# Kernel optimization log

Measured on AMD Instinct MI355X. Metric: run time of the kernel, lower is better.

Reference implementation:

```python
import jax, jax.numpy as jnp
import numpy as np

EMBED = 512; HEADS = 16; WIN = 8; SHIFT = 4

def _rel_pos_index(Wh, Ww):
    # WindowMSA.double_step_seq + transpose-sum + flip(1)
    seq1 = np.arange(0, (2 * Ww - 1) * Wh, 2 * Ww - 1)
    seq2 = np.arange(0, Ww)
    coords = (seq1[:, None] + seq2[None, :]).reshape(1, -1)
    idx = coords + coords.T            # (Wh*Ww, Wh*Ww)
    return idx[:, ::-1].copy()

def _attn_mask(H_pad, W_pad, win, shift, nf):
    # static (trace-time) shifted-window mask, values in {0, -100}
    img = np.zeros((H_pad, W_pad))
    cnt = 0
    for h in (slice(0, -win), slice(-win, -shift), slice(-shift, None)):
        for w in (slice(0, -win), slice(-win, -shift), slice(-shift, None)):
            img[h, w] = cnt
            cnt += 1
    mw = img.reshape(H_pad // win, win, W_pad // win, win).transpose(0, 2, 1, 3).reshape(-1, win * win)
    am = mw[:, None, :] - mw[:, :, None]
    am = np.where(am != 0, -100.0, 0.0)
    return np.tile(am, (1, 1, nf))     # (nW, N, nf*N)

def setup_inputs():
    key = jax.random.key(0)
    ks = jax.random.split(key, 8)
    B, H, W, C, nf = 8, 128, 128, EMBED, 2
    s = 0.02
    return {
        'q': jax.random.normal(ks[0], (B, H * W, C), jnp.float32),
        'kv': jax.random.normal(ks[1], (B, nf, H * W, C), jnp.float32),
        'H': H, 'W': W,
        'rpb_table': jax.random.normal(ks[2], ((2 * WIN - 1) ** 2, HEADS), jnp.float32) * s,
        'Wq': jax.random.normal(ks[3], (C, C), jnp.float32) * s,
        'bq': jnp.zeros((C,), jnp.float32),
        'Wkv': jax.random.normal(ks[4], (C, 2 * C), jnp.float32) * s,
        'bkv': jnp.zeros((2 * C,), jnp.float32),
        'Wo': jax.random.normal(ks[5], (C, C), jnp.float32) * s,
        'bo': jnp.zeros((C,), jnp.float32),
    }

def reference(q, kv, H, W, rpb_table, Wq, bq, Wkv, bkv, Wo, bo):
    B, L, C = q.shape
    nf = kv.shape[1]
    win, shift, heads = WIN, SHIFT, HEADS
    hd = C // heads
    scale = hd ** -0.5
    pad_b = (-H) % win
    pad_r = (-W) % win
    x = q.reshape(B, H, W, C)
    kvx = kv.reshape(B * nf, H, W, C)
    x = jnp.pad(x, ((0, 0), (0, pad_b), (0, pad_r), (0, 0)))
    kvx = jnp.pad(kvx, ((0, 0), (0, pad_b), (0, pad_r), (0, 0)))
    Hp, Wp = H + pad_b, W + pad_r
    nh, nw = Hp // win, Wp // win
    if shift > 0:
        x = jnp.roll(x, (-shift, -shift), (1, 2))
        kvx = jnp.roll(kvx, (-shift, -shift), (1, 2))
        mask = jnp.asarray(_attn_mask(Hp, Wp, win, shift, nf), q.dtype)
    else:
        mask = None
    Nq = win * win
    Nk = nf * Nq
    # window partition: (B, Hp, Wp, C) -> (B*nh*nw, Nq, C)
    qw = x.reshape(B, nh, win, nw, win, C).transpose(0, 1, 3, 2, 4, 5).reshape(B * nh * nw, Nq, C)
    # kv: (B*nf, Hp, Wp, C) -> (B*nh*nw, nf*Nq, C)
    kvw = kvx.reshape(B, nf, nh, win, nw, win, C).transpose(0, 2, 4, 1, 3, 5, 6).reshape(B * nh * nw, Nk, C)
    Bw = qw.shape[0]
    qh = (qw @ Wq + bq).reshape(Bw, Nq, heads, hd).transpose(0, 2, 1, 3) * scale
    kvp = (kvw @ Wkv + bkv).reshape(Bw, Nk, 2, heads, hd).transpose(2, 0, 3, 1, 4)
    kh, vh = kvp[0], kvp[1]
    attn = jnp.einsum('bhqd,bhkd->bhqk', qh, kh)
    rpi = jnp.asarray(_rel_pos_index(win, win).reshape(-1))
    rpb = rpb_table[rpi].reshape(Nq, Nq, heads).transpose(2, 0, 1)  # (heads, Nq, Nq)
    attn = attn + jnp.tile(rpb, (1, 1, nf))[None]
    if mask is not None:
        nW = mask.shape[0]
        attn = (attn.reshape(Bw // nW, nW, heads, Nq, Nk) + mask[None, :, None]).reshape(Bw, heads, Nq, Nk)
    attn = jax.nn.softmax(attn, axis=-1)
    ow = jnp.einsum('bhqk,bhkd->bqhd', attn, vh).reshape(Bw, Nq, C)
    ow = ow @ Wo + bo
    # window reverse
    x = ow.reshape(B, nh, nw, win, win, C).transpose(0, 1, 3, 2, 4, 5).reshape(B, Hp, Wp, C)
    if shift > 0:
        x = jnp.roll(x, (shift, shift), (1, 2))
    x = x[:, :H, :W, :].reshape(B, H * W, C)
    return x
```

## Files before the change

kernel.cpp:

```cpp
#include <hip/hip_runtime.h>

typedef unsigned short ushort_t;
typedef short bf16x8 __attribute__((ext_vector_type(8)));
typedef float f32x4 __attribute__((ext_vector_type(4)));

#define MFMA16(a, b, c) __builtin_amdgcn_mfma_f32_16x16x32_bf16(a, b, c, 0, 0, 0)

static __device__ __forceinline__ float bf2f(ushort_t u) {
  union { unsigned int i; float f; } v;
  v.i = ((unsigned int)u) << 16;
  return v.f;
}
static __device__ __forceinline__ ushort_t f2bf(float f) {
  union { float f; unsigned int i; } v;
  v.f = f;
  unsigned int u = v.i;
  u = u + 0x7fffu + ((u >> 16) & 1u);
  return (ushort_t)(u >> 16);
}
static __device__ __forceinline__ unsigned int cvtpk(float lo, float hi) {
  unsigned int r;
  asm("v_cvt_pk_bf16_f32 %0, %1, %2" : "=v"(r) : "v"(lo), "v"(hi));
  return r;
}

__global__ void ws_sentinel(float* out, unsigned long long ws) {
  if (blockIdx.x == 0 && threadIdx.x == 0)
    out[0] = 1.0e6f * (1.0f + (float)(ws >> 23));
}

__global__ __launch_bounds__(256) void wtrans(const float* __restrict__ in,
                                              ushort_t* __restrict__ out,
                                              int R, int C) {
  int idx = blockIdx.x * 256 + threadIdx.x;
  if (idx < R * C) {
    int r = idx / C, c = idx - r * C;
    out[c * R + r] = f2bf(in[idx]);
  }
}

template <bool AF32, bool CF32>
__global__ __launch_bounds__(256, 2) void gemm_bt(const void* __restrict__ Av,
                                                  const ushort_t* __restrict__ Bt,
                                                  const float* __restrict__ bias,
                                                  void* __restrict__ Cv,
                                                  int N, int Nt) {
  const int K = 512;
  __shared__ ushort_t As[128 * 32];
  __shared__ ushort_t Bs[128 * 32];
  const int t = threadIdx.x;
  const int l = t & 63;
  const int wv = t >> 6;
  const int wr = wv >> 1, wc = wv & 1;
  const int lrow = l & 15;
  const int lk = (l >> 4) * 8;

  const int bid = blockIdx.x;
  const int xcd = bid & 7;
  const int slot = bid >> 3;
  const int mt = xcd + 8 * (slot / Nt);
  const int nt = slot % Nt;
  const long m0 = (long)mt * 128;
  const int n0 = nt * 128;

  const ushort_t* Bb = Bt + (long)n0 * K;
  const int srow = t >> 2;
  const int sseg = t & 3;

  auto loadA8 = [&](long row, int kcol) -> bf16x8 {
    if constexpr (AF32) {
      const float* p = (const float*)Av + (m0 + row) * K + kcol;
      f32x4 a = *(const f32x4*)(p);
      f32x4 b = *(const f32x4*)(p + 4);
      union { unsigned int u[4]; bf16x8 v; } r;
      r.u[0] = cvtpk(a[0], a[1]);
      r.u[1] = cvtpk(a[2], a[3]);
      r.u[2] = cvtpk(b[0], b[1]);
      r.u[3] = cvtpk(b[2], b[3]);
      return r.v;
    } else {
      const ushort_t* p = (const ushort_t*)Av + (m0 + row) * K + kcol;
      return *(const bf16x8*)p;
    }
  };

  const f32x4 fz = {0.f, 0.f, 0.f, 0.f};
  f32x4 acc[4][4];
#pragma unroll
  for (int i = 0; i < 4; i++)
#pragma unroll
    for (int j = 0; j < 4; j++) acc[i][j] = fz;

  for (int kk = 0; kk < K; kk += 32) {
    bf16x8 ta0 = loadA8(srow, kk + sseg * 8);
    bf16x8 ta1 = loadA8(64 + srow, kk + sseg * 8);
    bf16x8 tb0 = *(const bf16x8*)(Bb + (long)srow * K + kk + sseg * 8);
    bf16x8 tb1 = *(const bf16x8*)(Bb + (long)(64 + srow) * K + kk + sseg * 8);
    __syncthreads();
    *(bf16x8*)&As[t * 8] = ta0;
    *(bf16x8*)&As[2048 + t * 8] = ta1;
    *(bf16x8*)&Bs[t * 8] = tb0;
    *(bf16x8*)&Bs[2048 + t * 8] = tb1;
    __syncthreads();
    bf16x8 af[4], bfr[4];
#pragma unroll
    for (int mi = 0; mi < 4; mi++)
      af[mi] = *(const bf16x8*)&As[(wr * 64 + mi * 16 + lrow) * 32 + lk];
#pragma unroll
    for (int ni = 0; ni < 4; ni++)
      bfr[ni] = *(const bf16x8*)&Bs[(wc * 64 + ni * 16 + lrow) * 32 + lk];
#pragma unroll
    for (int mi = 0; mi < 4; mi++)
#pragma unroll
      for (int ni = 0; ni < 4; ni++)
        acc[mi][ni] = MFMA16(af[mi], bfr[ni], acc[mi][ni]);
  }

#pragma unroll
  for (int mi = 0; mi < 4; mi++) {
    const long row0 = m0 + wr * 64 + mi * 16 + (l >> 4) * 4;
#pragma unroll
    for (int ni = 0; ni < 4; ni++) {
      const int col = n0 + wc * 64 + ni * 16 + lrow;
      const float bv = bias[col];
#pragma unroll
      for (int r = 0; r < 4; r++) {
        const float val = acc[mi][ni][r] + bv;
        if constexpr (CF32)
          ((float*)Cv)[(row0 + r) * N + col] = val;
        else
          ((ushort_t*)Cv)[(row0 + r) * N + col] = f2bf(val);
      }
    }
  }
}

__global__ __launch_bounds__(64, 1) void attn_k(const ushort_t* __restrict__ Qp,
                                                const ushort_t* __restrict__ KVp,
                                                const float* __restrict__ rpbt,
                                                ushort_t* __restrict__ Ao) {
  __shared__ ushort_t P[64 * 136];
  __shared__ ushort_t Vt[32 * 136];
  __shared__ float Ltab[225];
  const int l = threadIdx.x;
  const int wnd = blockIdx.x;
  const int h = blockIdx.y;
  const int b = wnd >> 8;
  const int wh = (wnd >> 4) & 15;
  const int ww = wnd & 15;
  for (int i = l; i < 225; i += 64) Ltab[i] = rpbt[i * 16 + h];

  const int lrow = l & 15;
  const int lq = l >> 4;
  const int lk = lq * 8;

  auto qrow = [&](int q) -> long {
    int i = q >> 3, j = q & 7;
    int ho = (wh * 8 + i + 4) & 127;
    int wo = (ww * 8 + j + 4) & 127;
    return (long)((b << 14) + (ho << 7) + wo);
  };
  auto kvrow = [&](int kp) -> long {
    int f = kp >> 6, m = kp & 63;
    int i = m >> 3, j = m & 7;
    int ho = (wh * 8 + i + 4) & 127;
    int wo = (ww * 8 + j + 4) & 127;
    return (long)(((b * 2 + f) << 14) + (ho << 7) + wo);
  };
  auto cnt_of = [&](int m) -> int {
    int hr = wh * 8 + (m >> 3), wr2 = ww * 8 + (m & 7);
    int rh = hr < 120 ? 0 : (hr < 124 ? 1 : 2);
    int rw = wr2 < 120 ? 0 : (wr2 < 124 ? 1 : 2);
    return rh * 3 + rw;
  };
  auto cvec = [](int m) -> int { return 15 * (m >> 3) + (m & 7); };

  const f32x4 fz = {0.f, 0.f, 0.f, 0.f};
  f32x4 s[4][8];
#pragma unroll
  for (int mi = 0; mi < 4; mi++)
#pragma unroll
    for (int ni = 0; ni < 8; ni++) s[mi][ni] = fz;

  bf16x8 af[4];
#pragma unroll
  for (int mi = 0; mi < 4; mi++)
    af[mi] = *(const bf16x8*)(Qp + qrow(mi * 16 + lrow) * 512 + h * 32 + lk);
#pragma unroll
  for (int ni = 0; ni < 8; ni++) {
    bf16x8 kf = *(const bf16x8*)(KVp + kvrow(ni * 16 + lrow) * 1024 + h * 32 + lk);
#pragma unroll
    for (int mi = 0; mi < 4; mi++) s[mi][ni] = MFMA16(af[mi], kf, s[mi][ni]);
  }

  __syncthreads();

  const float scale = 0.17677669529663687f;
#pragma unroll
  for (int mi = 0; mi < 4; mi++) {
#pragma unroll
    for (int r = 0; r < 4; r++) {
      const int q = mi * 16 + lq * 4 + r;
      const int cq = cnt_of(q);
      const int cqv = cvec(q);
      float mx = -3.0e38f;
#pragma unroll
      for (int ni = 0; ni < 8; ni++) {
        const int k63 = (ni * 16 + lrow) & 63;
        float v = s[mi][ni][r] * scale + Ltab[cqv + cvec(63 - k63)];
        if (cnt_of(k63) != cq) v -= 100.f;
        s[mi][ni][r] = v;
        mx = fmaxf(mx, v);
      }
      mx = fmaxf(mx, __shfl_xor(mx, 1));
      mx = fmaxf(mx, __shfl_xor(mx, 2));
      mx = fmaxf(mx, __shfl_xor(mx, 4));
      mx = fmaxf(mx, __shfl_xor(mx, 8));
      float sum = 0.f;
#pragma unroll
      for (int ni = 0; ni < 8; ni++) {
        float p = __expf(s[mi][ni][r] - mx);
        s[mi][ni][r] = p;
        sum += p;
      }
      sum += __shfl_xor(sum, 1);
      sum += __shfl_xor(sum, 2);
      sum += __shfl_xor(sum, 4);
      sum += __shfl_xor(sum, 8);
      const float inv = 1.f / sum;
#pragma unroll
      for (int ni = 0; ni < 8; ni++)
        P[q * 136 + ni * 16 + lrow] = f2bf(s[mi][ni][r] * inv);
    }
  }

#pragma unroll
  for (int kv2 = 0; kv2 < 2; kv2++) {
    const int kp = l * 2 + kv2;
    const ushort_t* src = KVp + kvrow(kp) * 1024 + 512 + h * 32;
    bf16x8 v0 = *(const bf16x8*)(src);
    bf16x8 v1 = *(const bf16x8*)(src + 8);
    bf16x8 v2 = *(const bf16x8*)(src + 16);
    bf16x8 v3 = *(const bf16x8*)(src + 24);
#pragma unroll
    for (int d = 0; d < 8; d++) {
      Vt[(d) * 136 + kp] = (ushort_t)v0[d];
      Vt[(8 + d) * 136 + kp] = (ushort_t)v1[d];
      Vt[(16 + d) * 136 + kp] = (ushort_t)v2[d];
      Vt[(24 + d) * 136 + kp] = (ushort_t)v3[d];
    }
  }
  __syncthreads();

  f32x4 o[4][2];
#pragma unroll
  for (int mi = 0; mi < 4; mi++) { o[mi][0] = fz; o[mi][1] = fz; }
#pragma unroll
  for (int ks = 0; ks < 4; ks++) {
    bf16x8 pf[4];
#pragma unroll
    for (int mi = 0; mi < 4; mi++)
      pf[mi] = *(const bf16x8*)&P[(mi * 16 + lrow) * 136 + ks * 32 + lk];
#pragma unroll
    for (int ni = 0; ni < 2; ni++) {
      bf16x8 vf = *(const bf16x8*)&Vt[(ni * 16 + lrow) * 136 + ks * 32 + lk];
#pragma unroll
      for (int mi = 0; mi < 4; mi++) o[mi][ni] = MFMA16(pf[mi], vf, o[mi][ni]);
    }
  }

#pragma unroll
  for (int mi = 0; mi < 4; mi++)
#pragma unroll
    for (int ni = 0; ni < 2; ni++)
#pragma unroll
      for (int r = 0; r < 4; r++) {
        const int q = mi * 16 + lq * 4 + r;
        Ao[qrow(q) * 512 + h * 32 + ni * 16 + lrow] = f2bf(o[mi][ni][r]);
      }
}

extern "C" void kernel_launch(void* const* d_in, const int* in_sizes, int n_in,
                              void* d_out, int out_size, void* d_ws, size_t ws_size,
                              hipStream_t stream) {
  (void)in_sizes; (void)n_in; (void)out_size;
  const float* q    = (const float*)d_in[0];
  const float* kv   = (const float*)d_in[1];
  const float* rpbt = (const float*)d_in[4];
  const float* Wq   = (const float*)d_in[5];
  const float* bq   = (const float*)d_in[6];
  const float* Wkv  = (const float*)d_in[7];
  const float* bkv  = (const float*)d_in[8];
  const float* Wo   = (const float*)d_in[9];
  const float* bo   = (const float*)d_in[10];
  float* out = (float*)d_out;

  const size_t QB  = 16384ULL * 512;
  const size_t KVB = 32768ULL * 1024;
  const size_t per_b_bytes = (QB + QB + KVB) * 2;
  const size_t fixed_bytes = (512ULL*512 + 512ULL*1024 + 512ULL*512) * 2;
  const size_t needed1 = fixed_bytes + per_b_bytes;

  if (ws_size < needed1) {
    ws_sentinel<<<dim3(1), 64, 0, stream>>>(out, (unsigned long long)ws_size);
    return;
  }

  int nbc = 8;
  while (nbc > 1 && fixed_bytes + (size_t)nbc * per_b_bytes > ws_size) nbc >>= 1;

  char* ws = (char*)d_ws;
  ushort_t* WqT  = (ushort_t*)ws;
  ushort_t* WkvT = WqT + 512 * 512;
  ushort_t* WoT  = WkvT + 512 * 1024;
  ushort_t* Qp   = (ushort_t*)(ws + fixed_bytes);
  ushort_t* Ao   = Qp + (size_t)nbc * QB;
  ushort_t* KVp  = Ao + (size_t)nbc * QB;

  wtrans<<<dim3(1024), 256, 0, stream>>>(Wq, WqT, 512, 512);
  wtrans<<<dim3(2048), 256, 0, stream>>>(Wkv, WkvT, 512, 1024);
  wtrans<<<dim3(1024), 256, 0, stream>>>(Wo, WoT, 512, 512);

  for (int c = 0; c < 8 / nbc; ++c) {
    const size_t b0 = (size_t)c * nbc;
    const int MtQ = nbc * 128;
    const int MtKV = nbc * 256;
    gemm_bt<true, false><<<dim3(MtQ * 4), 256, 0, stream>>>(q + b0 * QB, WqT, bq,
                                                            Qp, 512, 4);
    gemm_bt<true, false><<<dim3(MtKV * 8), 256, 0, stream>>>(kv + b0 * KVB / 2, WkvT,
                                                             bkv, KVp, 1024, 8);
    attn_k<<<dim3(nbc * 256, 16), 64, 0, stream>>>(Qp, KVp, rpbt, Ao);
    gemm_bt<false, true><<<dim3(MtQ * 4), 256, 0, stream>>>(Ao, WoT, bo,
                                                            out + b0 * QB, 512, 4);
  }
}
```

Measured before the change: 1.181 ms.

## Load GEMM tiles directly into LDS with global_load_lds and XOR swizzle

After: 1.095 ms. 1.08x faster.

```diff
diff --git a/kernel.cpp b/kernel.cpp
--- a/kernel.cpp
+++ b/kernel.cpp
@@ -22,6 +22,11 @@
   unsigned int r;
   asm("v_cvt_pk_bf16_f32 %0, %1, %2" : "=v"(r) : "v"(lo), "v"(hi));
   return r;
+}
+static __device__ __forceinline__ void gload16(const void* g, void* l) {
+  __builtin_amdgcn_global_load_lds((const __attribute__((address_space(1))) void*)g,
+                                   (__attribute__((address_space(3))) void*)l,
+                                   16, 0, 0);
 }
 
 __global__ void ws_sentinel(float* out, unsigned long long ws) {
@@ -45,15 +50,15 @@
                                                   const float* __restrict__ bias,
                                                   void* __restrict__ Cv,
                                                   int N, int Nt) {
-  const int K = 512;
-  __shared__ ushort_t As[128 * 32];
-  __shared__ ushort_t Bs[128 * 32];
+  constexpr int K = 512;
+  __shared__ unsigned char As[AF32 ? 128 * 32 * 4 : 128 * 32 * 2];
+  __shared__ unsigned char Bs[128 * 32 * 2];
   const int t = threadIdx.x;
   const int l = t & 63;
-  const int wv = t >> 6;
-  const int wr = wv >> 1, wc = wv & 1;
+  const int w = t >> 6;
+  const int w32 = w * 32;
+  const int wr = w >> 1, wc = w & 1;
   const int lrow = l & 15;
-  const int lk = (l >> 4) * 8;
 
   const int bid = blockIdx.x;
   const int xcd = bid & 7;
@@ -63,26 +68,10 @@
   const long m0 = (long)mt * 128;
   const int n0 = nt * 128;
 
-  const ushort_t* Bb = Bt + (long)n0 * K;
-  const int srow = t >> 2;
-  const int sseg = t & 3;
-
-  auto loadA8 = [&](long row, int kcol) -> bf16x8 {
-    if constexpr (AF32) {
-      const float* p = (const float*)Av + (m0 + row) * K + kcol;
-      f32x4 a = *(const f32x4*)(p);
-      f32x4 b = *(const f32x4*)(p + 4);
-      union { unsigned int u[4]; bf16x8 v; } r;
-      r.u[0] = cvtpk(a[0], a[1]);
-      r.u[1] = cvtpk(a[2], a[3]);
-      r.u[2] = cvtpk(b[0], b[1]);
-      r.u[3] = cvtpk(b[2], b[3]);
-      return r.v;
-    } else {
-      const ushort_t* p = (const ushort_t*)Av + (m0 + row) * K + kcol;
-      return *(const bf16x8*)p;
-    }
-  };
+  const int arow = l >> 3;
+  const int acol = ((16 * (l & 7)) ^ ((arow & 7) << 4)) >> 2;
+  const int brow = l >> 2;
+  const int bcol = ((16 * (l & 3)) ^ ((brow & 3) << 4)) >> 1;
 
   const f32x4 fz = {0.f, 0.f, 0.f, 0.f};
   f32x4 acc[4][4];
@@ -92,23 +81,55 @@
     for (int j = 0; j < 4; j++) acc[i][j] = fz;
 
   for (int kk = 0; kk < K; kk += 32) {
-    bf16x8 ta0 = loadA8(srow, kk + sseg * 8);
-    bf16x8 ta1 = loadA8(64 + srow, kk + sseg * 8);
-    bf16x8 tb0 = *(const bf16x8*)(Bb + (long)srow * K + kk + sseg * 8);
-    bf16x8 tb1 = *(const bf16x8*)(Bb + (long)(64 + srow) * K + kk + sseg * 8);
     __syncthreads();
-    *(bf16x8*)&As[t * 8] = ta0;
-    *(bf16x8*)&As[2048 + t * 8] = ta1;
-    *(bf16x8*)&Bs[t * 8] = tb0;
-    *(bf16x8*)&Bs[2048 + t * 8] = tb1;
+    if constexpr (AF32) {
+#pragma unroll
+      for (int i = 0; i < 4; i++) {
+        const float* g = (const float*)Av + (m0 + w32 + i * 8 + arow) * (long)K + kk + acol;
+        gload16(g, &As[(w32 + i * 8) * 128]);
+      }
+    } else {
+#pragma unroll
+      for (int i = 0; i < 2; i++) {
+        const ushort_t* g = (const ushort_t*)Av + (m0 + w32 + i * 16 + brow) * (long)K + kk + bcol;
+        gload16(g, &As[(w32 + i * 16) * 64]);
+      }
+    }
+#pragma unroll
+    for (int i = 0; i < 2; i++) {
+      const ushort_t* g = Bt + (long)(n0 + w32 + i * 16 + brow) * K + kk + bcol;
+      gload16(g, &Bs[(w32 + i * 16) * 64]);
+    }
     __syncthreads();
+
     bf16x8 af[4], bfr[4];
-#pragma unroll
-    for (int mi = 0; mi < 4; mi++)
-      af[mi] = *(const bf16x8*)&As[(wr * 64 + mi * 16 + lrow) * 32 + lk];
-#pragma unroll
-    for (int ni = 0; ni < 4; ni++)
-      bfr[ni] = *(const bf16x8*)&Bs[(wc * 64 + ni * 16 + lrow) * 32 + lk];
+    if constexpr (AF32) {
+#pragma unroll
+      for (int mi = 0; mi < 4; mi++) {
+        const int aR = wr * 64 + mi * 16 + lrow;
+        const int s = (aR & 7) << 4;
+        const int c0 = (l >> 4) * 32;
+        f32x4 x = *(const f32x4*)&As[aR * 128 + (c0 ^ s)];
+        f32x4 y = *(const f32x4*)&As[aR * 128 + ((c0 + 16) ^ s)];
+        union { unsigned int u[4]; bf16x8 v; } r;
+        r.u[0] = cvtpk(x[0], x[1]);
+        r.u[1] = cvtpk(x[2], x[3]);
+        r.u[2] = cvtpk(y[0], y[1]);
+        r.u[3] = cvtpk(y[2], y[3]);
+        af[mi] = r.v;
+      }
+    } else {
+#pragma unroll
+      for (int mi = 0; mi < 4; mi++) {
+        const int aR = wr * 64 + mi * 16 + lrow;
+        af[mi] = *(const bf16x8*)&As[aR * 64 + (((l >> 4) * 16) ^ ((aR & 3) << 4))];
+      }
+    }
+#pragma unroll
+    for (int ni = 0; ni < 4; ni++) {
+      const int bR = wc * 64 + ni * 16 + lrow;
+      bfr[ni] = *(const bf16x8*)&Bs[bR * 64 + (((l >> 4) * 16) ^ ((bR & 3) << 4))];
+    }
 #pragma unroll
     for (int mi = 0; mi < 4; mi++)
 #pragma unroll
```
